# Performance work log

Measured on AMD Instinct MI355X. Metric: run time of the kernel, lower is better.

Reference implementation:

```python
import jax, jax.numpy as jnp
import numpy as np

N = 100000   # nodes
E = 1600000  # edges (avg degree 16)
D = 64
L = 4        # layers per GNN stack


def setup_inputs() -> dict:
    key = jax.random.key(0)
    ks = jax.random.split(key, 16)
    s = 0.125  # ~kaiming scale for fan_in=64
    return {
        "x": jax.random.normal(ks[0], (N, D), jnp.float32),
        "edge_index": jax.random.randint(ks[1], (2, E), 0, N, dtype=jnp.int32),
        "sage_Wl": jax.random.normal(ks[2], (L, D, D), jnp.float32) * s,
        "sage_bl": jnp.zeros((L, D), jnp.float32),
        "sage_Wr": jax.random.normal(ks[3], (L, D, D), jnp.float32) * s,
        "gat_W": jax.random.normal(ks[4], (L, D, D), jnp.float32) * s,
        "gat_asrc": jax.random.normal(ks[5], (L, D), jnp.float32) * s,
        "gat_adst": jax.random.normal(ks[6], (L, D), jnp.float32) * s,
        "gat_b": jnp.zeros((L, D), jnp.float32),
        "proj_W1": jax.random.normal(ks[7], (64, 64), jnp.float32) * s,
        "proj_b1": jnp.zeros((64,), jnp.float32),
        "proj_W2": jax.random.normal(ks[8], (32, 64), jnp.float32) * s,
        "proj_b2": jnp.zeros((32,), jnp.float32),
        "proj_W3": jax.random.normal(ks[9], (16, 32), jnp.float32) * (0.25 ** 0.5),
        "proj_b3": jnp.zeros((16,), jnp.float32),
    }


def _sage_conv(x, Wl, bl, Wr, src, dst, n):
    # out_i = Wl @ mean_{j in N(i)} x_j + bl + Wr @ x_i
    msg_sum = jax.ops.segment_sum(x[src], dst, num_segments=n)
    deg = jax.ops.segment_sum(jnp.ones(src.shape[0], x.dtype), dst, num_segments=n)
    mean = msg_sum / jnp.maximum(deg, 1.0)[:, None]
    return mean @ Wl.T + bl + x @ Wr.T


def _gat_conv(x, W, a_src, a_dst, b, src_sl, dst_sl, n):
    # single-head GATConv with self-loops (src_sl/dst_sl include them)
    h = x @ W.T                      # [N, D]
    alpha_s = h @ a_src              # [N]
    alpha_d = h @ a_dst              # [N]
    e = jax.nn.leaky_relu(alpha_s[src_sl] + alpha_d[dst_sl], 0.2)  # [E+N]
    m = jax.ops.segment_max(e, dst_sl, num_segments=n)
    p = jnp.exp(e - m[dst_sl])
    z = jax.ops.segment_sum(p, dst_sl, num_segments=n)
    alpha = p / z[dst_sl]
    out = jax.ops.segment_sum(alpha[:, None] * h[src_sl], dst_sl, num_segments=n)
    return out + b


def reference(x, edge_index, sage_Wl, sage_bl, sage_Wr,
              gat_W, gat_asrc, gat_adst, gat_b,
              proj_W1, proj_b1, proj_W2, proj_b2, proj_W3, proj_b3):
    n = x.shape[0]
    src, dst = edge_index[0], edge_index[1]
    loops = jnp.arange(n, dtype=edge_index.dtype)
    src_sl = jnp.concatenate([src, loops])
    dst_sl = jnp.concatenate([dst, loops])

    h = x
    for i in range(L):  # GraphSAGE: ReLU between layers, none after last
        h = _sage_conv(h, sage_Wl[i], sage_bl[i], sage_Wr[i], src, dst, n)
        if i < L - 1:
            h = jax.nn.relu(h)
    for i in range(L):  # GAT
        h = _gat_conv(h, gat_W[i], gat_asrc[i], gat_adst[i], gat_b[i], src_sl, dst_sl, n)
        if i < L - 1:
            h = jax.nn.relu(h)

    # Projection MLP (Dropout inactive at inference)
    h = jax.nn.relu(h @ proj_W1.T + proj_b1)
    h = jax.nn.relu(h @ proj_W2.T + proj_b2)
    return h @ proj_W3.T + proj_b3
```

## Files before the change

kernel.cpp:

```cpp
#include <hip/hip_runtime.h>
#include <hip/hip_fp16.h>

#define D 64
#define D4 16
#define PITCH 68

typedef float4 f4;
typedef unsigned int u32;

__device__ __forceinline__ float leaky02(float x) { return (x >= 0.f) ? x : 0.2f * x; }

__device__ __forceinline__ f4 f4add(f4 a, f4 b) {
    return make_float4(a.x + b.x, a.y + b.y, a.z + b.z, a.w + b.w);
}
__device__ __forceinline__ f4 f4fma(float s, f4 v, f4 a) {
    return make_float4(fmaf(s, v.x, a.x), fmaf(s, v.y, a.y), fmaf(s, v.z, a.z), fmaf(s, v.w, a.w));
}
__device__ __forceinline__ f4 f4scale(f4 a, float s) {
    return make_float4(a.x * s, a.y * s, a.z * s, a.w * s);
}

__device__ __forceinline__ u32 pack2(float a, float b) {
    __half2 h = __floats2half2_rn(a, b);
    return *reinterpret_cast<u32*>(&h);
}
__device__ __forceinline__ uint2 pack4(float a, float b, float c, float d) {
    uint2 u;
    u.x = pack2(a, b);
    u.y = pack2(c, d);
    return u;
}
__device__ __forceinline__ f4 h2f4(uint2 u) {
    __half2 ha = *reinterpret_cast<__half2*>(&u.x);
    __half2 hb = *reinterpret_cast<__half2*>(&u.y);
    float2 fa = __half22float2(ha);
    float2 fb = __half22float2(hb);
    return make_float4(fa.x, fa.y, fb.x, fb.y);
}


__global__ __launch_bounds__(256) void hist_kernel(const int* __restrict__ dst,
                                                   int* __restrict__ cnt, int ne) {
    int e = blockIdx.x * blockDim.x + threadIdx.x;
    if (e < ne) atomicAdd(&cnt[dst[e]], 1);
}

#define SCAN_BS 256
__global__ __launch_bounds__(SCAN_BS) void scan1_kernel(const int* __restrict__ cnt,
                                                        int* __restrict__ incl,
                                                        int* __restrict__ partials, int n) {
    __shared__ int sm[SCAN_BS];
    int g = blockIdx.x * SCAN_BS + threadIdx.x;
    int v = (g < n) ? cnt[g] : 0;
    sm[threadIdx.x] = v;
    __syncthreads();
    for (int off = 1; off < SCAN_BS; off <<= 1) {
        int t = (threadIdx.x >= off) ? sm[threadIdx.x - off] : 0;
        __syncthreads();
        sm[threadIdx.x] += t;
        __syncthreads();
    }
    if (g < n) incl[g] = sm[threadIdx.x];
    if (threadIdx.x == SCAN_BS - 1) partials[blockIdx.x] = sm[threadIdx.x];
}

__global__ __launch_bounds__(1024) void scan2_kernel(int* __restrict__ partials, int nb) {
    __shared__ int sm[1024];
    int t = threadIdx.x;
    int v = (t < nb) ? partials[t] : 0;
    sm[t] = v;
    __syncthreads();
    for (int off = 1; off < 1024; off <<= 1) {
        int x = (t >= off) ? sm[t - off] : 0;
        __syncthreads();
        sm[t] += x;
        __syncthreads();
    }
    if (t < nb) partials[t] = sm[t] - v;
}

__global__ __launch_bounds__(SCAN_BS) void scan3_kernel(const int* __restrict__ cnt,
                                                        const int* __restrict__ incl,
                                                        const int* __restrict__ partials,
                                                        int* __restrict__ rowptr,
                                                        int* __restrict__ cursor, int n, int ne) {
    int g = blockIdx.x * SCAN_BS + threadIdx.x;
    if (g < n) {
        int rp = incl[g] - cnt[g] + partials[blockIdx.x];
        rowptr[g] = rp;
        cursor[g] = rp;
    }
    if (g == 0) rowptr[n] = ne;
}

__global__ __launch_bounds__(256) void fill_kernel(const int* __restrict__ src,
                                                   const int* __restrict__ dst,
                                                   int* __restrict__ cursor,
                                                   int* __restrict__ col, int ne) {
    int e = blockIdx.x * blockDim.x + threadIdx.x;
    if (e < ne) {
        int pos = atomicAdd(&cursor[dst[e]], 1);
        col[pos] = src[e];
    }
}


__global__ __launch_bounds__(256) void to_half(const float* __restrict__ in,
                                               uint2* __restrict__ out, int total4) {
    int i = blockIdx.x * 256 + threadIdx.x;
    if (i < total4) {
        f4 v = *(const f4*)&in[i * 4];
        out[i] = pack4(v.x, v.y, v.z, v.w);
    }
}


__device__ __forceinline__ void stageT(float* __restrict__ T, const f4* __restrict__ G4,
                                       int t, int valid_rows) {
    int row = t >> 2;
    int kq0 = t & 3;
#pragma unroll
    for (int c = 0; c < 4; c++) {
        int kq = kq0 + 4 * c;
        f4 r = make_float4(0.f, 0.f, 0.f, 0.f);
        if (row < valid_rows) r = G4[(size_t)row * 16 + kq];
        int k0 = kq * 4;
        T[(k0 + 0) * PITCH + row] = r.x;
        T[(k0 + 1) * PITCH + row] = r.y;
        T[(k0 + 2) * PITCH + row] = r.z;
        T[(k0 + 3) * PITCH + row] = r.w;
    }
}

#define TILE_MM(At, Wt, acc, r, c, KDIM)                                      \
    for (int k = 0; k < KDIM; k++) {                                          \
        f4 a = *(const f4*)&(At)[k * PITCH + (r) * 4];                        \
        f4 w = *(const f4*)&(Wt)[k * PITCH + (c) * 4];                        \
        acc[0][0] = fmaf(a.x, w.x, acc[0][0]);                                \
        acc[0][1] = fmaf(a.x, w.y, acc[0][1]);                                \
        acc[0][2] = fmaf(a.x, w.z, acc[0][2]);                                \
        acc[0][3] = fmaf(a.x, w.w, acc[0][3]);                                \
        acc[1][0] = fmaf(a.y, w.x, acc[1][0]);                                \
        acc[1][1] = fmaf(a.y, w.y, acc[1][1]);                                \
        acc[1][2] = fmaf(a.y, w.z, acc[1][2]);                                \
        acc[1][3] = fmaf(a.y, w.w, acc[1][3]);                                \
        acc[2][0] = fmaf(a.z, w.x, acc[2][0]);                                \
        acc[2][1] = fmaf(a.z, w.y, acc[2][1]);                                \
        acc[2][2] = fmaf(a.z, w.z, acc[2][2]);                                \
        acc[2][3] = fmaf(a.z, w.w, acc[2][3]);                                \
        acc[3][0] = fmaf(a.w, w.x, acc[3][0]);                                \
        acc[3][1] = fmaf(a.w, w.y, acc[3][1]);                                \
        acc[3][2] = fmaf(a.w, w.z, acc[3][2]);                                \
        acc[3][3] = fmaf(a.w, w.w, acc[3][3]);                                \
    }


__global__ __launch_bounds__(256) void sage_gather(const uint2* __restrict__ Hh,
                                                   const int* __restrict__ rowptr,
                                                   const int* __restrict__ col,
                                                   f4* __restrict__ M, int n) {
    int lane = threadIdx.x & 63;
    int eg = lane >> 4, l16 = lane & 15;
    int wave = (blockIdx.x * 256 + threadIdx.x) >> 6;
    int nw = (gridDim.x * 256) >> 6;
    for (int node = wave; node < n; node += nw) {
        int start = rowptr[node], end = rowptr[node + 1];
        int len = end - start;
        f4 a0 = {0, 0, 0, 0}, a1 = {0, 0, 0, 0}, a2 = {0, 0, 0, 0}, a3 = {0, 0, 0, 0};
        int main16 = len & ~15;
        int o = 0;
        for (; o < main16; o += 16) {
            int i0 = start + o + eg;
            int s0 = col[i0];
            int s1 = col[i0 + 4];
            int s2 = col[i0 + 8];
            int s3 = col[i0 + 12];
            uint2 v0 = Hh[(size_t)s0 * D4 + l16];
            uint2 v1 = Hh[(size_t)s1 * D4 + l16];
            uint2 v2 = Hh[(size_t)s2 * D4 + l16];
            uint2 v3 = Hh[(size_t)s3 * D4 + l16];
            a0 = f4add(a0, h2f4(v0)); a1 = f4add(a1, h2f4(v1));
            a2 = f4add(a2, h2f4(v2)); a3 = f4add(a3, h2f4(v3));
        }
        int rem = len - o;
        if (rem > 0) {
            int i0 = start + o;
            if (eg < rem)      a0 = f4add(a0, h2f4(Hh[(size_t)col[i0 + eg] * D4 + l16]));
            if (eg + 4 < rem)  a1 = f4add(a1, h2f4(Hh[(size_t)col[i0 + 4 + eg] * D4 + l16]));
            if (eg + 8 < rem)  a2 = f4add(a2, h2f4(Hh[(size_t)col[i0 + 8 + eg] * D4 + l16]));
            if (eg + 12 < rem) a3 = f4add(a3, h2f4(Hh[(size_t)col[i0 + 12 + eg] * D4 + l16]));
        }
        f4 a = f4add(f4add(a0, a1), f4add(a2, a3));
        a.x += __shfl_xor(a.x, 16); a.y += __shfl_xor(a.y, 16);
        a.z += __shfl_xor(a.z, 16); a.w += __shfl_xor(a.w, 16);
        a.x += __shfl_xor(a.x, 32); a.y += __shfl_xor(a.y, 32);
        a.z += __shfl_xor(a.z, 32); a.w += __shfl_xor(a.w, 32);
        if (eg == 0) {
            float invd = 1.f / fmaxf((float)len, 1.f);
            M[(size_t)node * D4 + l16] =
                make_float4(a.x * invd, a.y * invd, a.z * invd, a.w * invd);
        }
    }
}


__global__ __launch_bounds__(256) void sage_dense2(const f4* __restrict__ M4,
                                                   const f4* __restrict__ h4,
                                                   const float* __restrict__ Wl,
                                                   const float* __restrict__ bl,
                                                   const float* __restrict__ Wr,
                                                   f4* __restrict__ out4,
                                                   uint2* __restrict__ outh,
                                                   int relu_flag, int n) {
    __shared__ float At[64 * PITCH];
    __shared__ float Wt[64 * PITCH];
    int t = threadIdx.x;
    int nb = blockIdx.x * 64;
    int r = t >> 4, c = t & 15;
    float acc[4][4] = {{0.f}};
    stageT(At, M4 + (size_t)nb * 16, t, n - nb);
    stageT(Wt, (const f4*)Wl, t, 64);
    __syncthreads();
    TILE_MM(At, Wt, acc, r, c, 64)
    __syncthreads();
    stageT(At, h4 + (size_t)nb * 16, t, n - nb);
    stageT(Wt, (const f4*)Wr, t, 64);
    __syncthreads();
    TILE_MM(At, Wt, acc, r, c, 64)
    f4 bv = ((const f4*)bl)[c];
#pragma unroll
    for (int i = 0; i < 4; i++) {
        int node = nb + r * 4 + i;
        if (node < n) {
            f4 o = make_float4(acc[i][0] + bv.x, acc[i][1] + bv.y,
                               acc[i][2] + bv.z, acc[i][3] + bv.w);
            if (relu_flag) {
                o.x = fmaxf(o.x, 0.f); o.y = fmaxf(o.y, 0.f);
                o.z = fmaxf(o.z, 0.f); o.w = fmaxf(o.w, 0.f);
            }
            out4[(size_t)node * 16 + c] = o;
            outh[(size_t)node * 16 + c] = pack4(o.x, o.y, o.z, o.w);
        }
    }
}


__global__ __launch_bounds__(256) void gat_transform(const f4* __restrict__ h4,
                                                     const float* __restrict__ W,
                                                     const float* __restrict__ a_src,
                                                     const float* __restrict__ a_dst,
                                                     uint2* __restrict__ hth,
                                                     float* __restrict__ as_,
                                                     float* __restrict__ ad_, int n) {
    __shared__ float At[64 * PITCH];
    __shared__ float Wt[64 * PITCH];
    __shared__ float ps[16][68];
    __shared__ float pd[16][68];
    int t = threadIdx.x;
    int nb = blockIdx.x * 64;
    int r = t >> 4, c = t & 15;
    stageT(At, h4 + (size_t)nb * 16, t, n - nb);
    stageT(Wt, (const f4*)W, t, 64);
    __syncthreads();
    float acc[4][4] = {{0.f}};
    TILE_MM(At, Wt, acc, r, c, 64)
    f4 sv = ((const f4*)a_src)[c];
    f4 dv = ((const f4*)a_dst)[c];
#pragma unroll
    for (int i = 0; i < 4; i++) {
        int node = nb + r * 4 + i;
        if (node < n)
            hth[(size_t)node * 16 + c] = pack4(acc[i][0], acc[i][1], acc[i][2], acc[i][3]);
        ps[c][r * 4 + i] = acc[i][0] * sv.x + acc[i][1] * sv.y +
                           acc[i][2] * sv.z + acc[i][3] * sv.w;
        pd[c][r * 4 + i] = acc[i][0] * dv.x + acc[i][1] * dv.y +
                           acc[i][2] * dv.z + acc[i][3] * dv.w;
    }
    __syncthreads();
    if (t < 64) {
        int node = nb + t;
        if (node < n) {
            float s = 0.f, d = 0.f;
#pragma unroll
            for (int cc = 0; cc < 16; cc++) {
                s += ps[cc][t];
                d += pd[cc][t];
            }
            as_[node] = s;
            ad_[node] = d;
        }
    }
}


__global__ __launch_bounds__(256) void gat_gather(const int* __restrict__ rowptr,
                                                  const int* __restrict__ col,
                                                  const float* __restrict__ as_,
                                                  const float* __restrict__ ad_,
                                                  const uint2* __restrict__ Hh,
                                                  const float* __restrict__ b,
                                                  f4* __restrict__ out,
                                                  int relu_flag, int n) {
    int lane = threadIdx.x & 63;
    int eg = lane >> 4, l16 = lane & 15;
    int wave = (blockIdx.x * 256 + threadIdx.x) >> 6;
    int nw = (gridDim.x * 256) >> 6;
    const f4* b4 = (const f4*)b;
    for (int node = wave; node < n; node += nw) {
        int start = rowptr[node], end = rowptr[node + 1];
        int len = end - start;
        float ad_n = ad_[node];
        float e_self = leaky02(as_[node] + ad_n);
        float m = e_self;
        float zp = (eg == 0) ? 1.f : 0.f;
        f4 acc = {0, 0, 0, 0};
        if (eg == 0) acc = h2f4(Hh[(size_t)node * D4 + l16]);
        int main16 = len & ~15;
        int o = 0;
        for (; o < main16; o += 16) {
            int i0 = start + o + eg;
            int s0 = col[i0];
            int s1 = col[i0 + 4];
            int s2 = col[i0 + 8];
            int s3 = col[i0 + 12];
            uint2 v0 = Hh[(size_t)s0 * D4 + l16];
            uint2 v1 = Hh[(size_t)s1 * D4 + l16];
            uint2 v2 = Hh[(size_t)s2 * D4 + l16];
            uint2 v3 = Hh[(size_t)s3 * D4 + l16];
            float e0 = leaky02(as_[s0] + ad_n);
            float e1 = leaky02(as_[s1] + ad_n);
            float e2 = leaky02(as_[s2] + ad_n);
            float e3 = leaky02(as_[s3] + ad_n);
            float em = fmaxf(fmaxf(e0, e1), fmaxf(e2, e3));
            em = fmaxf(em, __shfl_xor(em, 16));
            em = fmaxf(em, __shfl_xor(em, 32));
            if (em > m) {
                float sc = __expf(m - em);
                zp *= sc;
                acc = f4scale(acc, sc);
                m = em;
            }
            float p0 = __expf(e0 - m);
            float p1 = __expf(e1 - m);
            float p2 = __expf(e2 - m);
            float p3 = __expf(e3 - m);
            zp += (p0 + p1) + (p2 + p3);
            acc = f4fma(p0, h2f4(v0), acc);
            acc = f4fma(p1, h2f4(v1), acc);
            acc = f4fma(p2, h2f4(v2), acc);
            acc = f4fma(p3, h2f4(v3), acc);
        }
        int rem = len - o;
        if (rem > 0) {
            int i0 = start + o;
            bool v0b = eg < rem, v1b = eg + 4 < rem, v2b = eg + 8 < rem, v3b = eg + 12 < rem;
            int s0 = v0b ? col[i0 + eg] : 0;
            int s1 = v1b ? col[i0 + 4 + eg] : 0;
            int s2 = v2b ? col[i0 + 8 + eg] : 0;
            int s3 = v3b ? col[i0 + 12 + eg] : 0;
            float e0 = v0b ? leaky02(as_[s0] + ad_n) : -3.4e38f;
            float e1 = v1b ? leaky02(as_[s1] + ad_n) : -3.4e38f;
            float e2 = v2b ? leaky02(as_[s2] + ad_n) : -3.4e38f;
            float e3 = v3b ? leaky02(as_[s3] + ad_n) : -3.4e38f;
            float em = fmaxf(fmaxf(e0, e1), fmaxf(e2, e3));
            em = fmaxf(em, __shfl_xor(em, 16));
            em = fmaxf(em, __shfl_xor(em, 32));
            if (em > m) {
                float sc = __expf(m - em);
                zp *= sc;
                acc = f4scale(acc, sc);
                m = em;
            }
            float p0 = v0b ? __expf(e0 - m) : 0.f;
            float p1 = v1b ? __expf(e1 - m) : 0.f;
            float p2 = v2b ? __expf(e2 - m) : 0.f;
            float p3 = v3b ? __expf(e3 - m) : 0.f;
            zp += (p0 + p1) + (p2 + p3);
            if (v0b) acc = f4fma(p0, h2f4(Hh[(size_t)s0 * D4 + l16]), acc);
            if (v1b) acc = f4fma(p1, h2f4(Hh[(size_t)s1 * D4 + l16]), acc);
            if (v2b) acc = f4fma(p2, h2f4(Hh[(size_t)s2 * D4 + l16]), acc);
            if (v3b) acc = f4fma(p3, h2f4(Hh[(size_t)s3 * D4 + l16]), acc);
        }
        float z = zp;
        z += __shfl_xor(z, 16);
        z += __shfl_xor(z, 32);
        acc.x += __shfl_xor(acc.x, 16); acc.y += __shfl_xor(acc.y, 16);
        acc.z += __shfl_xor(acc.z, 16); acc.w += __shfl_xor(acc.w, 16);
        acc.x += __shfl_xor(acc.x, 32); acc.y += __shfl_xor(acc.y, 32);
        acc.z += __shfl_xor(acc.z, 32); acc.w += __shfl_xor(acc.w, 32);
        if (eg == 0) {
            float rz = 1.f / z;
            f4 bb = b4[l16];
            f4 o4 = make_float4(fmaf(acc.x, rz, bb.x), fmaf(acc.y, rz, bb.y),
                                fmaf(acc.z, rz, bb.z), fmaf(acc.w, rz, bb.w));
            if (relu_flag) {
                o4.x = fmaxf(o4.x, 0.f); o4.y = fmaxf(o4.y, 0.f);
                o4.z = fmaxf(o4.z, 0.f); o4.w = fmaxf(o4.w, 0.f);
            }
            out[(size_t)node * D4 + l16] = o4;
        }
    }
}


__global__ __launch_bounds__(256) void mlp_kernel(const f4* __restrict__ h4,
                                                  const float* __restrict__ W1,
                                                  const float* __restrict__ b1,
                                                  const float* __restrict__ W2,
                                                  const float* __restrict__ b2,
                                                  const float* __restrict__ W3,
                                                  const float* __restrict__ b3,
                                                  float* __restrict__ out, int n) {
    __shared__ float At[64 * PITCH];
    __shared__ float Wt[64 * PITCH];
    __shared__ float V2[32 * PITCH];
    int t = threadIdx.x;
    int nb = blockIdx.x * 64;
    int r = t >> 4, c = t & 15;
    stageT(At, h4 + (size_t)nb * 16, t, n - nb);
    stageT(Wt, (const f4*)W1, t, 64);
    __syncthreads();
    float a1v[4][4] = {{0.f}};
    TILE_MM(At, Wt, a1v, r, c, 64)
    f4 b1v = ((const f4*)b1)[c];
    __syncthreads();
    {
        float bb[4] = {b1v.x, b1v.y, b1v.z, b1v.w};
#pragma unroll
        for (int i = 0; i < 4; i++)
#pragma unroll
            for (int j = 0; j < 4; j++)
                At[(c * 4 + j) * PITCH + r * 4 + i] = fmaxf(a1v[i][j] + bb[j], 0.f);
    }
    stageT(Wt, (const f4*)W2, t, 32);
    __syncthreads();
    float a2v[4][2] = {{0.f}};
    for (int k = 0; k < 64; k++) {
        f4 a = *(const f4*)&At[k * PITCH + r * 4];
        float w0 = Wt[k * PITCH + c * 2];
        float w1 = Wt[k * PITCH + c * 2 + 1];
        a2v[0][0] = fmaf(a.x, w0, a2v[0][0]); a2v[0][1] = fmaf(a.x, w1, a2v[0][1]);
        a2v[1][0] = fmaf(a.y, w0, a2v[1][0]); a2v[1][1] = fmaf(a.y, w1, a2v[1][1]);
        a2v[2][0] = fmaf(a.z, w0, a2v[2][0]); a2v[2][1] = fmaf(a.z, w1, a2v[2][1]);
        a2v[3][0] = fmaf(a.w, w0, a2v[3][0]); a2v[3][1] = fmaf(a.w, w1, a2v[3][1]);
    }
    float b20 = b2[c * 2], b21 = b2[c * 2 + 1];
    __syncthreads();
#pragma unroll
    for (int i = 0; i < 4; i++) {
        V2[(c * 2 + 0) * PITCH + r * 4 + i] = fmaxf(a2v[i][0] + b20, 0.f);
        V2[(c * 2 + 1) * PITCH + r * 4 + i] = fmaxf(a2v[i][1] + b21, 0.f);
    }
    if (t < 128) {
        int row = t >> 3, kq = t & 7;
        f4 w = ((const f4*)W3)[row * 8 + kq];
        int k0 = kq * 4;
        Wt[(k0 + 0) * PITCH + row] = w.x;
        Wt[(k0 + 1) * PITCH + row] = w.y;
        Wt[(k0 + 2) * PITCH + row] = w.z;
        Wt[(k0 + 3) * PITCH + row] = w.w;
    }
    __syncthreads();
    float a3v[4] = {0.f, 0.f, 0.f, 0.f};
    for (int k = 0; k < 32; k++) {
        f4 a = *(const f4*)&V2[k * PITCH + r * 4];
        float w = Wt[k * PITCH + c];
        a3v[0] = fmaf(a.x, w, a3v[0]);
        a3v[1] = fmaf(a.y, w, a3v[1]);
        a3v[2] = fmaf(a.z, w, a3v[2]);
        a3v[3] = fmaf(a.w, w, a3v[3]);
    }
    float b3v = b3[c];
#pragma unroll
    for (int i = 0; i < 4; i++) {
        int node = nb + r * 4 + i;
        if (node < n) out[(size_t)node * 16 + c] = a3v[i] + b3v;
    }
}


extern "C" void kernel_launch(void* const* d_in, const int* in_sizes, int n_in,
                              void* d_out, int out_size, void* d_ws, size_t ws_size,
                              hipStream_t stream) {
    const int n  = in_sizes[0] / D;
    const int ne = in_sizes[1] / 2;

    const float* x        = (const float*)d_in[0];
    const int*   ei       = (const int*)d_in[1];
    const int*   src      = ei;
    const int*   dst      = ei + ne;
    const float* sage_Wl  = (const float*)d_in[2];
    const float* sage_bl  = (const float*)d_in[3];
    const float* sage_Wr  = (const float*)d_in[4];
    const float* gat_W    = (const float*)d_in[5];
    const float* gat_asrc = (const float*)d_in[6];
    const float* gat_adst = (const float*)d_in[7];
    const float* gat_b    = (const float*)d_in[8];
    const float* W1 = (const float*)d_in[9];
    const float* b1 = (const float*)d_in[10];
    const float* W2 = (const float*)d_in[11];
    const float* b2 = (const float*)d_in[12];
    const float* W3 = (const float*)d_in[13];
    const float* b3 = (const float*)d_in[14];
    float* out = (float*)d_out;

    int*   cnt      = (int*)d_ws;
    int*   incl     = cnt + n;
    int*   rowptr   = incl + n;
    int*   cursor   = rowptr + n + 4;
    int*   partials = cursor + n;
    int*   col      = partials + 1024;
    float* as_      = (float*)(col + ne);
    float* ad_      = as_ + n;
    float* M        = ad_ + n;
    float* bufA     = M + (size_t)n * D;
    float* bufB     = bufA + (size_t)n * D;
    uint2* Hh       = (uint2*)(bufB + (size_t)n * D);

    const int gridE  = (ne + 255) / 256;
    const int nb     = (n + SCAN_BS - 1) / SCAN_BS;
    const int gridG  = 4096;
    const int gridM  = (n + 63) / 64;
    const int gridC  = (n * D / 4 + 255) / 256;

    hipMemsetAsync(cnt, 0, (size_t)n * 4, stream);
    hist_kernel<<<gridE, 256, 0, stream>>>(dst, cnt, ne);
    scan1_kernel<<<nb, SCAN_BS, 0, stream>>>(cnt, incl, partials, n);
    scan2_kernel<<<1, 1024, 0, stream>>>(partials, nb);
    scan3_kernel<<<nb, SCAN_BS, 0, stream>>>(cnt, incl, partials, rowptr, cursor, n, ne);
    fill_kernel<<<gridE, 256, 0, stream>>>(src, dst, cursor, col, ne);

    to_half<<<gridC, 256, 0, stream>>>(x, Hh, n * D / 4);
    const float* cur = x;
    float* nxt = bufA;
    for (int l = 0; l < 4; l++) {
        sage_gather<<<gridG, 256, 0, stream>>>(Hh, rowptr, col, (f4*)M, n);
        sage_dense2<<<gridM, 256, 0, stream>>>((const f4*)M, (const f4*)cur,
                                               sage_Wl + (size_t)l * D * D,
                                               sage_bl + (size_t)l * D,
                                               sage_Wr + (size_t)l * D * D,
                                               (f4*)nxt, Hh, (l < 3) ? 1 : 0, n);
        cur = nxt;
        nxt = (nxt == bufA) ? bufB : bufA;
    }

    float* gin = bufB;
    for (int l = 0; l < 4; l++) {
        gat_transform<<<gridM, 256, 0, stream>>>((const f4*)gin,
                                                 gat_W + (size_t)l * D * D,
                                                 gat_asrc + (size_t)l * D,
                                                 gat_adst + (size_t)l * D,
                                                 Hh, as_, ad_, n);
        gat_gather<<<gridG, 256, 0, stream>>>(rowptr, col, as_, ad_,
                                              Hh, gat_b + (size_t)l * D, (f4*)gin,
                                              (l < 3) ? 1 : 0, n);
    }

    mlp_kernel<<<gridM, 256, 0, stream>>>((const f4*)gin, W1, b1, W2, b2, W3, b3, out, n);
}
```

Measured before the change: 904.8 us.

## Use fp16 MFMA for SAGE dense and GAT transform matmuls

Replaces the scalar FP32 shared-memory tiled matmuls in the SAGE dense layer and the GAT transform with MFMA 16x16x16 fp16 instructions. Operands are converted to half and staged row-major in LDS, and results are written out through lane shuffles that pack pairs into half2. The GAT attention dot products are now reduced with wave shuffles instead of a shared-memory reduction. This trades matmul precision, since inputs become fp16 with fp32 accumulation, for less ALU work. The main cost is probably in the gathers, so the overall effect may be limited.

```diff
diff --git a/kernel.cpp b/kernel.cpp
--- a/kernel.cpp
+++ b/kernel.cpp
@@ -4,9 +4,12 @@
 #define D 64
 #define D4 16
 #define PITCH 68
+#define HP 36
 
 typedef float4 f4;
 typedef unsigned int u32;
+typedef __attribute__((ext_vector_type(4))) _Float16 f16x4;
+typedef __attribute__((ext_vector_type(4))) float f32x4;
 
 __device__ __forceinline__ float leaky02(float x) { return (x >= 0.f) ? x : 0.2f * x; }
 
@@ -112,6 +115,28 @@
         f4 v = *(const f4*)&in[i * 4];
         out[i] = pack4(v.x, v.y, v.z, v.w);
     }
+}
+
+
+__device__ __forceinline__ void stage_h32(u32* __restrict__ T, const f4* __restrict__ G4,
+                                          int t, int valid_rows) {
+    int row = t >> 2, q = t & 3;
+#pragma unroll
+    for (int c = 0; c < 4; c++) {
+        int kq = q + 4 * c;
+        f4 r = make_float4(0.f, 0.f, 0.f, 0.f);
+        if (row < valid_rows) r = G4[(size_t)row * 16 + kq];
+        uint2 p = pack4(r.x, r.y, r.z, r.w);
+        T[row * HP + kq * 2] = p.x;
+        T[row * HP + kq * 2 + 1] = p.y;
+    }
+}
+
+__device__ __forceinline__ f16x4 ldfrag(const u32* __restrict__ T, int row, int kidx) {
+    uint2 v;
+    v.x = T[row * HP + kidx * 2];
+    v.y = T[row * HP + kidx * 2 + 1];
+    return __builtin_bit_cast(f16x4, v);
 }
 
 
@@ -204,90 +229,124 @@
 }
 
 
-__global__ __launch_bounds__(256) void sage_dense2(const f4* __restrict__ M4,
-                                                   const f4* __restrict__ h4,
-                                                   const float* __restrict__ Wl,
-                                                   const float* __restrict__ bl,
-                                                   const float* __restrict__ Wr,
-                                                   f4* __restrict__ out4,
-                                                   uint2* __restrict__ outh,
-                                                   int relu_flag, int n) {
-    __shared__ float At[64 * PITCH];
-    __shared__ float Wt[64 * PITCH];
+__global__ __launch_bounds__(256) void sage_dense_mfma(const f4* __restrict__ M4,
+                                                       const f4* __restrict__ h4,
+                                                       const float* __restrict__ Wl,
+                                                       const float* __restrict__ bl,
+                                                       const float* __restrict__ Wr,
+                                                       float* __restrict__ outf,
+                                                       u32* __restrict__ outh32,
+                                                       int relu_flag, int n) {
+    __shared__ __align__(16) u32 Ah[64 * HP];
+    __shared__ __align__(16) u32 Bh[64 * HP];
     int t = threadIdx.x;
     int nb = blockIdx.x * 64;
-    int r = t >> 4, c = t & 15;
-    float acc[4][4] = {{0.f}};
-    stageT(At, M4 + (size_t)nb * 16, t, n - nb);
-    stageT(Wt, (const f4*)Wl, t, 64);
-    __syncthreads();
-    TILE_MM(At, Wt, acc, r, c, 64)
-    __syncthreads();
-    stageT(At, h4 + (size_t)nb * 16, t, n - nb);
-    stageT(Wt, (const f4*)Wr, t, 64);
-    __syncthreads();
-    TILE_MM(At, Wt, acc, r, c, 64)
-    f4 bv = ((const f4*)bl)[c];
-#pragma unroll
-    for (int i = 0; i < 4; i++) {
-        int node = nb + r * 4 + i;
-        if (node < n) {
-            f4 o = make_float4(acc[i][0] + bv.x, acc[i][1] + bv.y,
-                               acc[i][2] + bv.z, acc[i][3] + bv.w);
-            if (relu_flag) {
-                o.x = fmaxf(o.x, 0.f); o.y = fmaxf(o.y, 0.f);
-                o.z = fmaxf(o.z, 0.f); o.w = fmaxf(o.w, 0.f);
+    int w = t >> 6, l = t & 63;
+    int lr = l & 15, g = l >> 4;
+    f32x4 acc[4] = {{0, 0, 0, 0}, {0, 0, 0, 0}, {0, 0, 0, 0}, {0, 0, 0, 0}};
+    stage_h32(Ah, M4 + (size_t)nb * 16, t, n - nb);
+    stage_h32(Bh, (const f4*)Wl, t, 64);
+    __syncthreads();
+#pragma unroll
+    for (int kb = 0; kb < 4; kb++) {
+        f16x4 af = ldfrag(Ah, w * 16 + lr, kb * 4 + g);
+#pragma unroll
+        for (int ob = 0; ob < 4; ob++) {
+            f16x4 bf = ldfrag(Bh, ob * 16 + lr, kb * 4 + g);
+            acc[ob] = __builtin_amdgcn_mfma_f32_16x16x16f16(af, bf, acc[ob], 0, 0, 0);
+        }
+    }
+    __syncthreads();
+    stage_h32(Ah, h4 + (size_t)nb * 16, t, n - nb);
+    stage_h32(Bh, (const f4*)Wr, t, 64);
+    __syncthreads();
+#pragma unroll
+    for (int kb = 0; kb < 4; kb++) {
+        f16x4 af = ldfrag(Ah, w * 16 + lr, kb * 4 + g);
+#pragma unroll
+        for (int ob = 0; ob < 4; ob++) {
+            f16x4 bf = ldfrag(Bh, ob * 16 + lr, kb * 4 + g);
+            acc[ob] = __builtin_amdgcn_mfma_f32_16x16x16f16(af, bf, acc[ob], 0, 0, 0);
+        }
+    }
+#pragma unroll
+    for (int ob = 0; ob < 4; ob++) {
+        int colx = ob * 16 + lr;
+        float bv = bl[colx];
+#pragma unroll
+        for (int j = 0; j < 4; j++) {
+            int row = w * 16 + 4 * g + j;
+            int node = nb + row;
+            float v = acc[ob][j] + bv;
+            if (relu_flag) v = fmaxf(v, 0.f);
+            float vup = __shfl_down(v, 1);
+            if (node < n) {
+                outf[(size_t)node * 64 + colx] = v;
+                if ((lr & 1) == 0) outh32[(size_t)node * 32 + (colx >> 1)] = pack2(v, vup);
             }
-            out4[(size_t)node * 16 + c] = o;
-            outh[(size_t)node * 16 + c] = pack4(o.x, o.y, o.z, o.w);
-        }
-    }
-}
-
-
-__global__ __launch_bounds__(256) void gat_transform(const f4* __restrict__ h4,
-                                                     const float* __restrict__ W,
-                                                     const float* __restrict__ a_src,
-                                                     const float* __restrict__ a_dst,
-                                                     uint2* __restrict__ hth,
-                                                     float* __restrict__ as_,
-                                                     float* __restrict__ ad_, int n) {
-    __shared__ float At[64 * PITCH];
-    __shared__ float Wt[64 * PITCH];
-    __shared__ float ps[16][68];
-    __shared__ float pd[16][68];
+        }
+    }
+}
+
+
+__global__ __launch_bounds__(256) void gat_transform_mfma(const f4* __restrict__ h4,
+                                                          const float* __restrict__ W,
+                                                          const float* __restrict__ a_src,
+                                                          const float* __restrict__ a_dst,
+                                                          u32* __restrict__ hth32,
+                                                          float* __restrict__ as_,
+                                                          float* __restrict__ ad_, int n) {
+    __shared__ __align__(16) u32 Ah[64 * HP];
+    __shared__ __align__(16) u32 Bh[64 * HP];
     int t = threadIdx.x;
     int nb = blockIdx.x * 64;
-    int r = t >> 4, c = t & 15;
-    stageT(At, h4 + (size_t)nb * 16, t, n - nb);
-    stageT(Wt, (const f4*)W, t, 64);
-    __syncthreads();
-    float acc[4][4] = {{0.f}};
-    TILE_MM(At, Wt, acc, r, c, 64)
-    f4 sv = ((const f4*)a_src)[c];
-    f4 dv = ((const f4*)a_dst)[c];
-#pragma unroll
-    for (int i = 0; i < 4; i++) {
-        int node = nb + r * 4 + i;
-        if (node < n)
-            hth[(size_t)node * 16 + c] = pack4(acc[i][0], acc[i][1], acc[i][2], acc[i][3]);
-        ps[c][r * 4 + i] = acc[i][0] * sv.x + acc[i][1] * sv.y +
-                           acc[i][2] * sv.z + acc[i][3] * sv.w;
-        pd[c][r * 4 + i] = acc[i][0] * dv.x + acc[i][1] * dv.y +
-                           acc[i][2] * dv.z + acc[i][3] * dv.w;
-    }
-    __syncthreads();
-    if (t < 64) {
-        int node = nb + t;
-        if (node < n) {
-            float s = 0.f, d = 0.f;
-#pragma unroll
-            for (int cc = 0; cc < 16; cc++) {
-                s += ps[cc][t];
-                d += pd[cc][t];
-            }
-            as_[node] = s;
-            ad_[node] = d;
+    int w = t >> 6, l = t & 63;
+    int lr = l & 15, g = l >> 4;
+    f32x4 acc[4] = {{0, 0, 0, 0}, {0, 0, 0, 0}, {0, 0, 0, 0}, {0, 0, 0, 0}};
+    stage_h32(Ah, h4 + (size_t)nb * 16, t, n - nb);
+    stage_h32(Bh, (const f4*)W, t, 64);
+    __syncthreads();
+#pragma unroll
+    for (int kb = 0; kb < 4; kb++) {
+        f16x4 af = ldfrag(Ah, w * 16 + lr, kb * 4 + g);
+#pragma unroll
+        for (int ob = 0; ob < 4; ob++) {
+            f16x4 bf = ldfrag(Bh, ob * 16 + lr, kb * 4 + g);
+            acc[ob] = __builtin_amdgcn_mfma_f32_16x16x16f16(af, bf, acc[ob], 0, 0, 0);
+        }
+    }
+    float asv[4], adv[4];
+#pragma unroll
+    for (int ob = 0; ob < 4; ob++) {
+        asv[ob] = a_src[ob * 16 + lr];
+        adv[ob] = a_dst[ob * 16 + lr];
+    }
+#pragma unroll
+    for (int j = 0; j < 4; j++) {
+        int row = w * 16 + 4 * g + j;
+        int node = nb + row;
+        float ps = 0.f, pd = 0.f;
+#pragma unroll
+        for (int ob = 0; ob < 4; ob++) {
+            ps = fmaf(acc[ob][j], asv[ob], ps);
+            pd = fmaf(acc[ob][j], adv[ob], pd);
+        }
+#pragma unroll
+        for (int off = 1; off < 16; off <<= 1) {
+            ps += __shfl_xor(ps, off);
+            pd += __shfl_xor(pd, off);
+        }
+        if (lr == 0 && node < n) {
+            as_[node] = ps;
+            ad_[node] = pd;
+        }
+#pragma unroll
+        for (int ob = 0; ob < 4; ob++) {
+            int colx = ob * 16 + lr;
+            float v = acc[ob][j];
+            float vup = __shfl_down(v, 1);
+            if (node < n && (lr & 1) == 0)
+                hth32[(size_t)node * 32 + (colx >> 1)] = pack2(v, vup);
         }
     }
 }
@@ -535,22 +594,22 @@
     float* nxt = bufA;
     for (int l = 0; l < 4; l++) {
         sage_gather<<<gridG, 256, 0, stream>>>(Hh, rowptr, col, (f4*)M, n);
-        sage_dense2<<<gridM, 256, 0, stream>>>((const f4*)M, (const f4*)cur,
-                                               sage_Wl + (size_t)l * D * D,
-                                               sage_bl + (size_t)l * D,
-                                               sage_Wr + (size_t)l * D * D,
-                                               (f4*)nxt, Hh, (l < 3) ? 1 : 0, n);
+        sage_dense_mfma<<<gridM, 256, 0, stream>>>((const f4*)M, (const f4*)cur,
+                                                   sage_Wl + (size_t)l * D * D,
+                                                   sage_bl + (size_t)l * D,
+                                                   sage_Wr + (size_t)l * D * D,
+                                                   nxt, (u32*)Hh, (l < 3) ? 1 : 0, n);
         cur = nxt;
         nxt = (nxt == bufA) ? bufB : bufA;
     }
 
     float* gin = bufB;
     for (int l = 0; l < 4; l++) {
-        gat_transform<<<gridM, 256, 0, stream>>>((const f4*)gin,
-                                                 gat_W + (size_t)l * D * D,
-                                                 gat_asrc + (size_t)l * D,
-                                                 gat_adst + (size_t)l * D,
-                                                 Hh, as_, ad_, n);
+        gat_transform_mfma<<<gridM, 256, 0, stream>>>((const f4*)gin,
+                                                      gat_W + (size_t)l * D * D,
+                                                      gat_asrc + (size_t)l * D,
+                                                      gat_adst + (size_t)l * D,
+                                                      (u32*)Hh, as_, ad_, n);
         gat_gather<<<gridG, 256, 0, stream>>>(rowptr, col, as_, ad_,
                                               Hh, gat_b + (size_t)l * D, (f4*)gin,
                                               (l < 3) ? 1 : 0, n);
```

Result: faster. 869.0 us, median of 2 (-4.0%).
